# Kernel optimization log

Measured on AMD Instinct MI355X. Metric: run time of the kernel, lower is better.

Reference implementation:

```python
import jax, jax.numpy as jnp
import numpy as np

B, S, D, N, LAYERS = 512, 64, 256, 100000, 1


def setup_inputs() -> dict:
    key = jax.random.key(0)
    ks = jax.random.split(key, 9)
    stdv = 1.0 / np.sqrt(D)
    return {
        "embedding": jax.random.uniform(ks[0], (N, D), jnp.float32, -stdv, stdv),
        "W1": jax.random.uniform(ks[1], (2 * D, 2 * D), jnp.float32, -stdv, stdv),
        "W2": jax.random.uniform(ks[2], (2 * D, D), jnp.float32, -stdv, stdv),
        "adj_in": jax.random.uniform(ks[3], (B, S, S), jnp.float32),
        "adj_out": jax.random.uniform(ks[4], (B, S, S), jnp.float32),
        "mask": jnp.ones((B, S), jnp.float32),
        "item": jax.random.randint(ks[5], (B, S), 0, N),
        "alias": jax.random.randint(ks[6], (B, S), 0, S),
        "tar": jax.random.randint(ks[7], (B,), 1, N),  # targets in [1, n_node)
    }


def reference(embedding, W1, W2, adj_in, adj_out, mask, item, alias, tar):
    # ---- sgc(): gather -> dual adjacency aggregation -> concat -> 2-layer MLP
    fin = embedding[item]                              # [B,S,D]
    # torch `adj ** layers` is elementwise power (not matrix power)
    fs_in = jnp.matmul(adj_in ** LAYERS, fin)          # [B,S,D]
    fs_out = jnp.matmul(adj_out ** LAYERS, fin)        # [B,S,D]
    av = jnp.concatenate([fs_in, fs_out], axis=-1)     # [B,S,2D]
    av = jnp.matmul(jax.nn.relu(jnp.matmul(av, W1)), W2)  # [B,S,D]

    # ---- forward(): pick last node's hidden, score against item table
    rows = jnp.arange(B)
    rm = jnp.sum(mask, axis=1).astype(jnp.int32)       # session lengths [B]
    last_id = alias[rows, rm - 1]                      # [B]
    last_h = av[rows, last_id]                         # [B,D]
    logits = last_h @ embedding[1:].T                  # [B,N-1]

    logp = jax.nn.log_softmax(logits, axis=-1)
    loss = -jnp.mean(logp[rows, tar - 1])
    # L2 term is zero: params live in a plain dict (not registered) and l2=0.
    return loss, logits
```

## Files before the change

kernel.cpp:

```cpp
#include <hip/hip_runtime.h>
#include <hip/hip_bf16.h>
#include <cstdint>
#include <cstddef>

#define BDIM 512
#define SDIM 64
#define DDIM 256
#define D2   512
#define NNODE 100000
#define NM1  99999

typedef short short8 __attribute__((ext_vector_type(8)));
typedef float f32x4 __attribute__((ext_vector_type(4)));

__device__ __forceinline__ unsigned short f2bf(float f) {
  unsigned int u = __float_as_uint(f);
  u += 0x7FFFu + ((u >> 16) & 1u);
  return (unsigned short)(u >> 16);
}

__global__ __launch_bounds__(256) void prep_kernel(
    const float* __restrict__ emb, const float* __restrict__ adj_in,
    const float* __restrict__ adj_out, const float* __restrict__ mask,
    const int* __restrict__ item, const int* __restrict__ alias_,
    float* __restrict__ av) {
  __shared__ float a_in[SDIM], a_out[SDIM];
  __shared__ int it[SDIM];
  __shared__ int s_star;
  const int b = blockIdx.x, t = threadIdx.x;
  if (t < SDIM) it[t] = item[b * SDIM + t];
  if (t == 0) {
    float s = 0.f;
    for (int j = 0; j < SDIM; j++) s += mask[b * SDIM + j];
    int rm = (int)s;
    s_star = alias_[b * SDIM + rm - 1];
  }
  __syncthreads();
  const int ss = s_star;
  if (t < SDIM) a_in[t] = adj_in[((size_t)b * SDIM + ss) * SDIM + t];
  else if (t < 2 * SDIM) a_out[t - SDIM] = adj_out[((size_t)b * SDIM + ss) * SDIM + (t - SDIM)];
  __syncthreads();
  const int d = t;
  float ai = 0.f, ao = 0.f;
#pragma unroll 8
  for (int j = 0; j < SDIM; j++) {
    float e = emb[(size_t)it[j] * DDIM + d];
    ai = fmaf(a_in[j], e, ai);
    ao = fmaf(a_out[j], e, ao);
  }
  av[(size_t)b * D2 + d] = ai;
  av[(size_t)b * D2 + DDIM + d] = ao;
}

__global__ __launch_bounds__(256) void mlp1_kernel(
    const float* __restrict__ A, const float* __restrict__ W,
    float* __restrict__ O) {
  __shared__ float As[16][16];
  __shared__ float Bs[16][17];
  const int tx = threadIdx.x, ty = threadIdx.y;
  const int row = blockIdx.y * 16 + ty, col = blockIdx.x * 16 + tx;
  float acc = 0.f;
  for (int k0 = 0; k0 < D2; k0 += 16) {
    As[ty][tx] = A[(size_t)row * D2 + k0 + tx];
    Bs[ty][tx] = W[(size_t)(k0 + ty) * D2 + col];
    __syncthreads();
#pragma unroll
    for (int k = 0; k < 16; k++) acc = fmaf(As[ty][k], Bs[k][tx], acc);
    __syncthreads();
  }
  O[(size_t)row * D2 + col] = fmaxf(acc, 0.f);
}

__global__ __launch_bounds__(256) void mlp2_kernel(
    const float* __restrict__ A, const float* __restrict__ W,
    unsigned short* __restrict__ O) {
  __shared__ float As[16][16];
  __shared__ float Bs[16][17];
  const int tx = threadIdx.x, ty = threadIdx.y;
  const int row = blockIdx.y * 16 + ty, col = blockIdx.x * 16 + tx;
  float acc = 0.f;
  for (int k0 = 0; k0 < D2; k0 += 16) {
    As[ty][tx] = A[(size_t)row * D2 + k0 + tx];
    Bs[ty][tx] = W[(size_t)(k0 + ty) * DDIM + col];
    __syncthreads();
#pragma unroll
    for (int k = 0; k < 16; k++) acc = fmaf(As[ty][k], Bs[k][tx], acc);
    __syncthreads();
  }
  O[(size_t)row * DDIM + col] = f2bf(acc);
}

#define LDA 72
__global__ __launch_bounds__(256) void logits_gemm(
    const unsigned short* __restrict__ Abf,
    const float* __restrict__ emb,
    float* __restrict__ out,
    float* __restrict__ rse) {
  __shared__ short As[128 * LDA];
  __shared__ short Bs[128 * LDA];
  const int t = threadIdx.x;
  const int mbase = blockIdx.x * 128;
  const int nbase = blockIdx.y * 128;
  const int lane = t & 63, w = t >> 6;
  const int wm = (w >> 1) * 64, wn = (w & 1) * 64;
  const int c = lane & 15, q = lane >> 4;

  f32x4 acc[4][4];
#pragma unroll
  for (int mi = 0; mi < 4; mi++)
#pragma unroll
    for (int ni = 0; ni < 4; ni++) acc[mi][ni] = (f32x4){0.f, 0.f, 0.f, 0.f};

  const int r8 = t >> 3;
  const int kcol = (t & 7) * 8;

  for (int k0 = 0; k0 < DDIM; k0 += 64) {
    __syncthreads();
#pragma unroll
    for (int i = 0; i < 4; i++) {
      const int row = i * 32 + r8;
      const short8 a8 = *(const short8*)(Abf + (size_t)(mbase + row) * DDIM + k0 + kcol);
      *(short8*)&As[row * LDA + kcol] = a8;
      const int n = nbase + row;
      const int er = (n + 1 <= NM1) ? (n + 1) : NM1;
      const float* bg = emb + (size_t)er * DDIM + k0 + kcol;
      const float4 b0 = *(const float4*)bg;
      const float4 b1 = *(const float4*)(bg + 4);
      short8 p;
      p[0] = (short)f2bf(b0.x); p[1] = (short)f2bf(b0.y);
      p[2] = (short)f2bf(b0.z); p[3] = (short)f2bf(b0.w);
      p[4] = (short)f2bf(b1.x); p[5] = (short)f2bf(b1.y);
      p[6] = (short)f2bf(b1.z); p[7] = (short)f2bf(b1.w);
      *(short8*)&Bs[row * LDA + kcol] = p;
    }
    __syncthreads();
#pragma unroll
    for (int kk = 0; kk < 64; kk += 32) {
      short8 afr[4], bfr[4];
#pragma unroll
      for (int mi = 0; mi < 4; mi++)
        afr[mi] = *(const short8*)&As[(wm + mi * 16 + c) * LDA + kk + q * 8];
#pragma unroll
      for (int ni = 0; ni < 4; ni++)
        bfr[ni] = *(const short8*)&Bs[(wn + ni * 16 + c) * LDA + kk + q * 8];
#pragma unroll
      for (int mi = 0; mi < 4; mi++)
#pragma unroll
        for (int ni = 0; ni < 4; ni++)
          acc[mi][ni] = __builtin_amdgcn_mfma_f32_16x16x32_bf16(
              afr[mi], bfr[ni], acc[mi][ni], 0, 0, 0);
    }
  }

#pragma unroll
  for (int mi = 0; mi < 4; mi++) {
#pragma unroll
    for (int r = 0; r < 4; r++) {
      const int grow = mbase + wm + mi * 16 + q * 4 + r;
      float s = 0.f;
#pragma unroll
      for (int ni = 0; ni < 4; ni++) {
        const int col = nbase + wn + ni * 16 + c;
        if (col < NM1) {
          const float v = acc[mi][ni][r];
          out[1 + (size_t)grow * NM1 + col] = v;
          s += __expf(v);
        }
      }
#pragma unroll
      for (int msk = 1; msk < 16; msk <<= 1) s += __shfl_xor(s, msk, 64);
      if (c == 0) atomicAdd(&rse[grow], s);
    }
  }
}

__global__ __launch_bounds__(512) void loss_kernel(
    float* __restrict__ out, const float* __restrict__ rse,
    const int* __restrict__ tar) {
  __shared__ float red[512];
  const int t = threadIdx.x;
  const int tt = tar[t];
  const float lg = out[1 + (size_t)t * NM1 + (tt - 1)];
  red[t] = logf(rse[t]) - lg;
  __syncthreads();
  for (int stride = 256; stride > 0; stride >>= 1) {
    if (t < stride) red[t] += red[t + stride];
    __syncthreads();
  }
  if (t == 0) out[0] = red[0] / (float)BDIM;
}

extern "C" void kernel_launch(void* const* d_in, const int* in_sizes, int n_in,
                              void* d_out, int out_size, void* d_ws, size_t ws_size,
                              hipStream_t stream) {
  const float* emb     = (const float*)d_in[0];
  const float* W1      = (const float*)d_in[1];
  const float* W2      = (const float*)d_in[2];
  const float* adj_in  = (const float*)d_in[3];
  const float* adj_out = (const float*)d_in[4];
  const float* mask    = (const float*)d_in[5];
  const int*   item    = (const int*)d_in[6];
  const int*   alias_  = (const int*)d_in[7];
  const int*   tar     = (const int*)d_in[8];
  float* out = (float*)d_out;

  char* ws = (char*)d_ws;
  float* av            = (float*)(ws);
  float* h1            = (float*)(ws + 1048576);
  unsigned short* lasth = (unsigned short*)(ws + 2097152);
  float* rse           = (float*)(ws + 2359296);

  hipMemsetAsync(rse, 0, BDIM * sizeof(float), stream);
  prep_kernel<<<BDIM, 256, 0, stream>>>(emb, adj_in, adj_out, mask, item, alias_, av);
  mlp1_kernel<<<dim3(32, 32), dim3(16, 16), 0, stream>>>(av, W1, h1);
  mlp2_kernel<<<dim3(16, 32), dim3(16, 16), 0, stream>>>(h1, W2, lasth);
  logits_gemm<<<dim3(4, 782), 256, 0, stream>>>(lasth, emb, out, rse);
  loss_kernel<<<1, 512, 0, stream>>>(out, rse, tar);
}
```

Before: 511.0 us.

## Fuse prep and MLP into one kernel; restructure logits GEMM to load embeddings once

The gather/aggregation, both MLP layers and the bf16 conversion now run in one per-session kernel, with intermediates kept in shared memory. This removes two launches and the global round trips for av and h1. The logits GEMM now gives each block 64 embedding rows converted to bf16 once and loops over all 512 batch rows. Each embedding row is therefore read and converted once instead of four times. The A operand is read straight from global memory (L2), with no LDS staging. The per-session MLP re-reads the whole of W1 and W2 in every block and has less parallelism than the tiled GEMMs.

```diff
diff --git a/kernel.cpp b/kernel.cpp
--- a/kernel.cpp
+++ b/kernel.cpp
@@ -19,14 +19,17 @@
   return (unsigned short)(u >> 16);
 }
 
-__global__ __launch_bounds__(256) void prep_kernel(
-    const float* __restrict__ emb, const float* __restrict__ adj_in,
+__global__ __launch_bounds__(256) void fused_mlp(
+    const float* __restrict__ emb, const float* __restrict__ W1,
+    const float* __restrict__ W2, const float* __restrict__ adj_in,
     const float* __restrict__ adj_out, const float* __restrict__ mask,
     const int* __restrict__ item, const int* __restrict__ alias_,
-    float* __restrict__ av) {
+    unsigned short* __restrict__ lasth) {
   __shared__ float a_in[SDIM], a_out[SDIM];
   __shared__ int it[SDIM];
   __shared__ int s_star;
+  __shared__ float av[D2];
+  __shared__ float h1[D2];
   const int b = blockIdx.x, t = threadIdx.x;
   if (t < SDIM) it[t] = item[b * SDIM + t];
   if (t == 0) {
@@ -40,109 +43,88 @@
   if (t < SDIM) a_in[t] = adj_in[((size_t)b * SDIM + ss) * SDIM + t];
   else if (t < 2 * SDIM) a_out[t - SDIM] = adj_out[((size_t)b * SDIM + ss) * SDIM + (t - SDIM)];
   __syncthreads();
-  const int d = t;
-  float ai = 0.f, ao = 0.f;
+  {
+    float ai = 0.f, ao = 0.f;
 #pragma unroll 8
-  for (int j = 0; j < SDIM; j++) {
-    float e = emb[(size_t)it[j] * DDIM + d];
-    ai = fmaf(a_in[j], e, ai);
-    ao = fmaf(a_out[j], e, ao);
+    for (int j = 0; j < SDIM; j++) {
+      float e = emb[(size_t)it[j] * DDIM + t];
+      ai = fmaf(a_in[j], e, ai);
+      ao = fmaf(a_out[j], e, ao);
+    }
+    av[t] = ai;
+    av[DDIM + t] = ao;
   }
-  av[(size_t)b * D2 + d] = ai;
-  av[(size_t)b * D2 + DDIM + d] = ao;
+  __syncthreads();
+  {
+    float acc0 = 0.f, acc1 = 0.f;
+#pragma unroll 4
+    for (int k = 0; k < D2; k++) {
+      const float a = av[k];
+      acc0 = fmaf(a, W1[(size_t)k * D2 + t], acc0);
+      acc1 = fmaf(a, W1[(size_t)k * D2 + t + 256], acc1);
+    }
+    h1[t] = fmaxf(acc0, 0.f);
+    h1[t + 256] = fmaxf(acc1, 0.f);
+  }
+  __syncthreads();
+  {
+    float acc = 0.f;
+#pragma unroll 4
+    for (int k = 0; k < D2; k++)
+      acc = fmaf(h1[k], W2[(size_t)k * DDIM + t], acc);
+    lasth[(size_t)b * DDIM + t] = f2bf(acc);
+  }
 }
 
-__global__ __launch_bounds__(256) void mlp1_kernel(
-    const float* __restrict__ A, const float* __restrict__ W,
-    float* __restrict__ O) {
-  __shared__ float As[16][16];
-  __shared__ float Bs[16][17];
-  const int tx = threadIdx.x, ty = threadIdx.y;
-  const int row = blockIdx.y * 16 + ty, col = blockIdx.x * 16 + tx;
-  float acc = 0.f;
-  for (int k0 = 0; k0 < D2; k0 += 16) {
-    As[ty][tx] = A[(size_t)row * D2 + k0 + tx];
-    Bs[ty][tx] = W[(size_t)(k0 + ty) * D2 + col];
-    __syncthreads();
-#pragma unroll
-    for (int k = 0; k < 16; k++) acc = fmaf(As[ty][k], Bs[k][tx], acc);
-    __syncthreads();
-  }
-  O[(size_t)row * D2 + col] = fmaxf(acc, 0.f);
-}
-
-__global__ __launch_bounds__(256) void mlp2_kernel(
-    const float* __restrict__ A, const float* __restrict__ W,
-    unsigned short* __restrict__ O) {
-  __shared__ float As[16][16];
-  __shared__ float Bs[16][17];
-  const int tx = threadIdx.x, ty = threadIdx.y;
-  const int row = blockIdx.y * 16 + ty, col = blockIdx.x * 16 + tx;
-  float acc = 0.f;
-  for (int k0 = 0; k0 < D2; k0 += 16) {
-    As[ty][tx] = A[(size_t)row * D2 + k0 + tx];
-    Bs[ty][tx] = W[(size_t)(k0 + ty) * DDIM + col];
-    __syncthreads();
-#pragma unroll
-    for (int k = 0; k < 16; k++) acc = fmaf(As[ty][k], Bs[k][tx], acc);
-    __syncthreads();
-  }
-  O[(size_t)row * DDIM + col] = f2bf(acc);
-}
-
-#define LDA 72
+#define LDB 264
 __global__ __launch_bounds__(256) void logits_gemm(
     const unsigned short* __restrict__ Abf,
     const float* __restrict__ emb,
     float* __restrict__ out,
     float* __restrict__ rse) {
-  __shared__ short As[128 * LDA];
-  __shared__ short Bs[128 * LDA];
+  __shared__ short Bs[64 * LDB];
   const int t = threadIdx.x;
-  const int mbase = blockIdx.x * 128;
-  const int nbase = blockIdx.y * 128;
-  const int lane = t & 63, w = t >> 6;
-  const int wm = (w >> 1) * 64, wn = (w & 1) * 64;
+  const int nbase = blockIdx.x * 64;
+
+#pragma unroll
+  for (int pass = 0; pass < 8; ++pass) {
+    const int g = pass * 512 + t * 2;
+    const int row = g >> 6;
+    const int c4 = g & 63;
+    int er = nbase + row + 1; if (er > NM1) er = NM1;
+    const float* bg = emb + (size_t)er * DDIM + c4 * 4;
+    const float4 b0 = ((const float4*)bg)[0];
+    const float4 b1 = ((const float4*)bg)[1];
+    short8 p;
+    p[0] = (short)f2bf(b0.x); p[1] = (short)f2bf(b0.y);
+    p[2] = (short)f2bf(b0.z); p[3] = (short)f2bf(b0.w);
+    p[4] = (short)f2bf(b1.x); p[5] = (short)f2bf(b1.y);
+    p[6] = (short)f2bf(b1.z); p[7] = (short)f2bf(b1.w);
+    *(short8*)&Bs[row * LDB + c4 * 4] = p;
+  }
+  __syncthreads();
+
+  const int w = t >> 6, lane = t & 63;
   const int c = lane & 15, q = lane >> 4;
 
-  f32x4 acc[4][4];
 #pragma unroll
-  for (int mi = 0; mi < 4; mi++)
+  for (int cc = 0; cc < 2; ++cc) {
+    const int arow0 = w * 128 + cc * 64;
+    f32x4 acc[4][4];
 #pragma unroll
-    for (int ni = 0; ni < 4; ni++) acc[mi][ni] = (f32x4){0.f, 0.f, 0.f, 0.f};
+    for (int mi = 0; mi < 4; mi++)
+#pragma unroll
+      for (int ni = 0; ni < 4; ni++) acc[mi][ni] = (f32x4){0.f, 0.f, 0.f, 0.f};
 
-  const int r8 = t >> 3;
-  const int kcol = (t & 7) * 8;
-
-  for (int k0 = 0; k0 < DDIM; k0 += 64) {
-    __syncthreads();
 #pragma unroll
-    for (int i = 0; i < 4; i++) {
-      const int row = i * 32 + r8;
-      const short8 a8 = *(const short8*)(Abf + (size_t)(mbase + row) * DDIM + k0 + kcol);
-      *(short8*)&As[row * LDA + kcol] = a8;
-      const int n = nbase + row;
-      const int er = (n + 1 <= NM1) ? (n + 1) : NM1;
-      const float* bg = emb + (size_t)er * DDIM + k0 + kcol;
-      const float4 b0 = *(const float4*)bg;
-      const float4 b1 = *(const float4*)(bg + 4);
-      short8 p;
-      p[0] = (short)f2bf(b0.x); p[1] = (short)f2bf(b0.y);
-      p[2] = (short)f2bf(b0.z); p[3] = (short)f2bf(b0.w);
-      p[4] = (short)f2bf(b1.x); p[5] = (short)f2bf(b1.y);
-      p[6] = (short)f2bf(b1.z); p[7] = (short)f2bf(b1.w);
-      *(short8*)&Bs[row * LDA + kcol] = p;
-    }
-    __syncthreads();
-#pragma unroll
-    for (int kk = 0; kk < 64; kk += 32) {
+    for (int kk = 0; kk < DDIM; kk += 32) {
       short8 afr[4], bfr[4];
 #pragma unroll
       for (int mi = 0; mi < 4; mi++)
-        afr[mi] = *(const short8*)&As[(wm + mi * 16 + c) * LDA + kk + q * 8];
+        afr[mi] = *(const short8*)(Abf + (size_t)(arow0 + mi * 16 + c) * DDIM + kk + q * 8);
 #pragma unroll
       for (int ni = 0; ni < 4; ni++)
-        bfr[ni] = *(const short8*)&Bs[(wn + ni * 16 + c) * LDA + kk + q * 8];
+        bfr[ni] = *(const short8*)&Bs[(ni * 16 + c) * LDB + kk + q * 8];
 #pragma unroll
       for (int mi = 0; mi < 4; mi++)
 #pragma unroll
@@ -150,26 +132,26 @@
           acc[mi][ni] = __builtin_amdgcn_mfma_f32_16x16x32_bf16(
               afr[mi], bfr[ni], acc[mi][ni], 0, 0, 0);
     }
-  }
 
 #pragma unroll
-  for (int mi = 0; mi < 4; mi++) {
+    for (int mi = 0; mi < 4; mi++) {
 #pragma unroll
-    for (int r = 0; r < 4; r++) {
-      const int grow = mbase + wm + mi * 16 + q * 4 + r;
-      float s = 0.f;
+      for (int r = 0; r < 4; r++) {
+        const int grow = arow0 + mi * 16 + q * 4 + r;
+        float s = 0.f;
 #pragma unroll
-      for (int ni = 0; ni < 4; ni++) {
-        const int col = nbase + wn + ni * 16 + c;
-        if (col < NM1) {
-          const float v = acc[mi][ni][r];
-          out[1 + (size_t)grow * NM1 + col] = v;
-          s += __expf(v);
+        for (int ni = 0; ni < 4; ni++) {
+          const int col = nbase + ni * 16 + c;
+          if (col < NM1) {
+            const float v = acc[mi][ni][r];
+            out[1 + (size_t)grow * NM1 + col] = v;
+            s += __expf(v);
+          }
         }
+#pragma unroll
+        for (int msk = 1; msk < 16; msk <<= 1) s += __shfl_xor(s, msk, 64);
+        if (c == 0) atomicAdd(&rse[grow], s);
       }
-#pragma unroll
-      for (int msk = 1; msk < 16; msk <<= 1) s += __shfl_xor(s, msk, 64);
-      if (c == 0) atomicAdd(&rse[grow], s);
     }
   }
 }
@@ -205,15 +187,12 @@
   float* out = (float*)d_out;
 
   char* ws = (char*)d_ws;
-  float* av            = (float*)(ws);
-  float* h1            = (float*)(ws + 1048576);
-  unsigned short* lasth = (unsigned short*)(ws + 2097152);
-  float* rse           = (float*)(ws + 2359296);
+  unsigned short* lasth = (unsigned short*)(ws);
+  float* rse            = (float*)(ws + 262144);
 
   hipMemsetAsync(rse, 0, BDIM * sizeof(float), stream);
-  prep_kernel<<<BDIM, 256, 0, stream>>>(emb, adj_in, adj_out, mask, item, alias_, av);
-  mlp1_kernel<<<dim3(32, 32), dim3(16, 16), 0, stream>>>(av, W1, h1);
-  mlp2_kernel<<<dim3(16, 32), dim3(16, 16), 0, stream>>>(h1, W2, lasth);
-  logits_gemm<<<dim3(4, 782), 256, 0, stream>>>(lasth, emb, out, rse);
+  fused_mlp<<<BDIM, 256, 0, stream>>>(emb, W1, W2, adj_in, adj_out, mask,
+                                      item, alias_, lasth);
+  logits_gemm<<<dim3((NM1 + 63) / 64), 256, 0, stream>>>(lasth, emb, out, rse);
   loss_kernel<<<1, 512, 0, stream>>>(out, rse, tar);
 }
```

Result: slower. 633.1 us (+23.9%).
